# Performance work log

Hardware: AMD Instinct MI355X
Metric: run time of the kernel (lower is better)

## Reference

```python
import jax, jax.numpy as jnp
import numpy as np
import math

B, S, D = 1, 4096, 2048
H, KVH, HD = 16, 4, 128
ROPE_THETA = 10000.0


def _rope_tables(seq_len, head_dim, theta):
    inv_freq = 1.0 / (theta ** (jnp.arange(0, head_dim, 2, dtype=jnp.float32) / head_dim))
    t = jnp.arange(seq_len, dtype=jnp.float32)
    freqs = jnp.outer(t, inv_freq)                      # [S, HD/2]
    emb = jnp.concatenate([freqs, freqs], axis=-1)      # [S, HD]
    return jnp.cos(emb)[None, None], jnp.sin(emb)[None, None]  # [1,1,S,HD]


def setup_inputs() -> dict:
    key = jax.random.key(0)
    ks = jax.random.split(key, 8)
    hidden_states = jax.random.normal(ks[0], (B, S, D), dtype=jnp.float32)
    # additive causal mask [B,1,S,S]
    neg = jnp.finfo(jnp.float32).min
    causal = jnp.where(jnp.tril(jnp.ones((S, S), dtype=bool)), 0.0, neg)
    attention_mask = jnp.broadcast_to(causal[None, None], (B, 1, S, S)).astype(jnp.float32)
    cos, sin = _rope_tables(S, HD, ROPE_THETA)
    gate = jax.random.uniform(ks[1], (B, S), dtype=jnp.float32, minval=0.05, maxval=1.0)
    sc = lambda fan_in: 1.0 / math.sqrt(fan_in)
    Wq = jax.random.normal(ks[2], (D, H * HD), dtype=jnp.float32) * sc(D)
    Wk = jax.random.normal(ks[3], (D, KVH * HD), dtype=jnp.float32) * sc(D)
    Wv = jax.random.normal(ks[4], (D, KVH * HD), dtype=jnp.float32) * sc(D)
    Wo = jax.random.normal(ks[5], (H * HD, D), dtype=jnp.float32) * sc(H * HD)
    return {"hidden_states": hidden_states, "attention_mask": attention_mask,
            "cos": cos, "sin": sin, "gate": gate,
            "Wq": Wq, "Wk": Wk, "Wv": Wv, "Wo": Wo}


def _rotate_half(x):
    h = x.shape[-1] // 2
    return jnp.concatenate([-x[..., h:], x[..., :h]], axis=-1)


def reference(hidden_states, attention_mask, cos, sin, gate, Wq, Wk, Wv, Wo):
    bsz, q_len, _ = hidden_states.shape
    # projections -> [B, heads, S, HD]
    q = (hidden_states @ Wq).reshape(bsz, q_len, H, HD).transpose(0, 2, 1, 3)
    k = (hidden_states @ Wk).reshape(bsz, q_len, KVH, HD).transpose(0, 2, 1, 3)
    v = (hidden_states @ Wv).reshape(bsz, q_len, KVH, HD).transpose(0, 2, 1, 3)
    # inline RoPE
    q = q * cos + _rotate_half(q) * sin
    k = k * cos + _rotate_half(k) * sin
    # GQA: repeat-interleave kv heads to match q heads
    g = H // KVH
    k = jnp.repeat(k, g, axis=1)
    v = jnp.repeat(v, g, axis=1)
    scores = jnp.einsum('bhqd,bhkd->bhqk', q, k) / math.sqrt(HD)
    scores = scores + attention_mask
    scores = scores + jnp.log(gate + 1e-8)[:, None, None, :]  # gate over kv positions
    weights = jax.nn.softmax(scores.astype(jnp.float32), axis=-1).astype(q.dtype)
    out = jnp.einsum('bhqk,bhkd->bhqd', weights, v)
    out = out.transpose(0, 2, 1, 3).reshape(bsz, q_len, H * HD)
    return out @ Wo
```

## Files before the change

kernel.cpp:

```cpp
#include <hip/hip_runtime.h>
#include <math.h>

#define S_LEN 4096
#define DMODEL 2048
#define NH 16
#define NKVH 4
#define HD 128
#define LDQKV 3072

typedef __attribute__((ext_vector_type(4))) float f32x4;
typedef __attribute__((ext_vector_type(8))) short bf16x8;
typedef __attribute__((ext_vector_type(4))) unsigned short us4;

static __device__ __forceinline__ unsigned short f2bf(float f) {
  unsigned int u = __builtin_bit_cast(unsigned int, f);
  u += 0x7fffu + ((u >> 16) & 1u);
  return (unsigned short)(u >> 16);
}
static __device__ __forceinline__ float bf2f(unsigned short h) {
  unsigned int u = ((unsigned int)h) << 16;
  return __builtin_bit_cast(float, u);
}
static __device__ __forceinline__ unsigned int cvt_pk_bf16(float lo, float hi) {
  unsigned int r;
  asm("v_cvt_pk_bf16_f32 %0, %1, %2" : "=v"(r) : "v"(lo), "v"(hi));
  return r;
}

#define GLDS16(g, l) __builtin_amdgcn_global_load_lds( \
    (__attribute__((address_space(1))) void*)(g), \
    (__attribute__((address_space(3))) void*)(l), 16, 0, 0)


__global__ __launch_bounds__(256) void k_cast_bf16(const float* __restrict__ src,
                                                   unsigned short* __restrict__ dst, int n4) {
  int i = blockIdx.x * 256 + threadIdx.x;
  if (i >= n4) return;
  const float4* s = (const float4*)src;
  float4 v = s[i];
  us4 o = { f2bf(v.x), f2bf(v.y), f2bf(v.z), f2bf(v.w) };
  *(us4*)(dst + (size_t)i * 4) = o;
}

__global__ __launch_bounds__(256) void k_transpose_w(
    const float* __restrict__ Wq, const float* __restrict__ Wk,
    const float* __restrict__ Wv, const float* __restrict__ Wo,
    unsigned short* __restrict__ Wt, unsigned short* __restrict__ Wot) {
  __shared__ float tile[64][65];
  const int b = blockIdx.x;
  const float* src;
  unsigned short* dst;
  int N, c;
  if (b < 1024)      { src = Wq; dst = Wt;                         N = 2048; c = b; }
  else if (b < 1280) { src = Wk; dst = Wt + (size_t)2048 * 2048;   N = 512;  c = b - 1024; }
  else if (b < 1536) { src = Wv; dst = Wt + (size_t)2560 * 2048;   N = 512;  c = b - 1280; }
  else               { src = Wo; dst = Wot;                        N = 2048; c = b - 1536; }
  const int k0 = (c & 31) * 64, n0 = (c >> 5) * 64;
  const int t = threadIdx.x;
#pragma unroll
  for (int i = 0; i < 16; ++i) {
    int idx = t + i * 256;
    int r = idx >> 6, cc = idx & 63;
    tile[r][cc] = src[(size_t)(k0 + r) * N + n0 + cc];
  }
  __syncthreads();
#pragma unroll
  for (int i = 0; i < 16; ++i) {
    int idx = t + i * 256;
    int r = idx >> 6, cc = idx & 63;
    dst[(size_t)(n0 + r) * 2048 + k0 + cc] = f2bf(tile[cc][r]);
  }
}

__global__ __launch_bounds__(256) void k_rope_tv(unsigned short* __restrict__ QKV,
    const float* __restrict__ cp, const float* __restrict__ sp,
    unsigned short* __restrict__ Vt) {
  __shared__ unsigned short tile[64][72];
  const int b = blockIdx.x, t = threadIdx.x;
  if (b < 5120) {
    int gid = b * 256 + t;
    int d4 = (gid & 15) * 4;
    int hh = (gid >> 4) % 20;
    int s = gid / 320;
    int col = hh < NH ? hh * HD : DMODEL + (hh - NH) * HD;
    float qs = hh < NH ? 0.12751589341664477f : 1.0f;
    size_t base = (size_t)s * LDQKV + col + d4;
    us4 x1 = *(us4*)(QKV + base);
    us4 x2 = *(us4*)(QKV + base + 64);
    float4 c = *(const float4*)(cp + s * HD + d4);
    float4 sn = *(const float4*)(sp + s * HD + d4);
    us4 o1, o2;
    o1[0] = f2bf((bf2f(x1[0]) * c.x - bf2f(x2[0]) * sn.x) * qs);
    o1[1] = f2bf((bf2f(x1[1]) * c.y - bf2f(x2[1]) * sn.y) * qs);
    o1[2] = f2bf((bf2f(x1[2]) * c.z - bf2f(x2[2]) * sn.z) * qs);
    o1[3] = f2bf((bf2f(x1[3]) * c.w - bf2f(x2[3]) * sn.w) * qs);
    o2[0] = f2bf((bf2f(x2[0]) * c.x + bf2f(x1[0]) * sn.x) * qs);
    o2[1] = f2bf((bf2f(x2[1]) * c.y + bf2f(x1[1]) * sn.y) * qs);
    o2[2] = f2bf((bf2f(x2[2]) * c.z + bf2f(x1[2]) * sn.z) * qs);
    o2[3] = f2bf((bf2f(x2[3]) * c.w + bf2f(x1[3]) * sn.w) * qs);
    *(us4*)(QKV + base) = o1;
    *(us4*)(QKV + base + 64) = o2;
  } else {
    const int bb = b - 5120;
    const int s0 = (bb & 63) * 64, c0 = (bb >> 6) * 64;
#pragma unroll
    for (int i = 0; i < 16; ++i) {
      int idx = t + i * 256;
      int r = idx >> 6, cc = idx & 63;
      tile[r][cc] = QKV[(size_t)(s0 + r) * LDQKV + DMODEL + NKVH * HD + c0 + cc];
    }
    __syncthreads();
#pragma unroll
    for (int i = 0; i < 16; ++i) {
      int idx = t + i * 256;
      int r = idx >> 6, cc = idx & 63;
      int pc = (cc & 3) * 16 + (cc >> 2);
      Vt[(size_t)(c0 + r) * S_LEN + s0 + cc] = tile[pc][r];
    }
  }
}


template<int OUTF32>
__global__ __launch_bounds__(256) void k_gemm_bt(
    const unsigned short* __restrict__ A, const unsigned short* __restrict__ Bt,
    void* __restrict__ Cp, int M, int N, int K) {
  __shared__ __attribute__((aligned(16))) unsigned short As[128 * 32];
  __shared__ __attribute__((aligned(16))) unsigned short Bs[128 * 32];
  const int t = threadIdx.x;
  const int wave = t >> 6, lane = t & 63;
  const int lr = lane & 15, lg = lane >> 4;
  const int bm = blockIdx.x * 128, bn = blockIdx.y * 128;
  const int wr = (wave >> 1) * 64, wc = (wave & 1) * 64;
  f32x4 acc[4][4];
#pragma unroll
  for (int i = 0; i < 4; ++i)
#pragma unroll
    for (int j = 0; j < 4; ++j) acc[i][j] = (f32x4){0.f, 0.f, 0.f, 0.f};

  for (int k0 = 0; k0 < K; k0 += 32) {
    __syncthreads();
#pragma unroll
    for (int i = 0; i < 2; ++i) {
      const int cb = (wave * 2 + i) * 64;
      const int c = cb + lane;
      const int row = c >> 2, kc = c & 3;
      const int ksw = (kc ^ (row & 3)) * 8;
      GLDS16(A + (size_t)(bm + row) * K + k0 + ksw, (char*)As + cb * 16);
      GLDS16(Bt + (size_t)(bn + row) * K + k0 + ksw, (char*)Bs + cb * 16);
    }
    asm volatile("s_waitcnt vmcnt(0)" ::: "memory");
    __syncthreads();
    bf16x8 af[4], bfr[4];
#pragma unroll
    for (int mi = 0; mi < 4; ++mi) {
      const int row = wr + mi * 16 + lr;
      af[mi] = *(const bf16x8*)(As + row * 32 + ((lg ^ (lr & 3)) * 8));
    }
#pragma unroll
    for (int ni = 0; ni < 4; ++ni) {
      const int row = wc + ni * 16 + lr;
      bfr[ni] = *(const bf16x8*)(Bs + row * 32 + ((lg ^ (lr & 3)) * 8));
    }
#pragma unroll
    for (int mi = 0; mi < 4; ++mi)
#pragma unroll
      for (int ni = 0; ni < 4; ++ni)
        acc[mi][ni] = __builtin_amdgcn_mfma_f32_16x16x32_bf16(af[mi], bfr[ni], acc[mi][ni], 0, 0, 0);
  }
#pragma unroll
  for (int mi = 0; mi < 4; ++mi)
#pragma unroll
    for (int ni = 0; ni < 4; ++ni)
#pragma unroll
      for (int r = 0; r < 4; ++r) {
        const int m = bm + wr + mi * 16 + lg * 4 + r;
        const int n = bn + wc + ni * 16 + lr;
        if (OUTF32) ((float*)Cp)[(size_t)m * N + n] = acc[mi][ni][r];
        else ((unsigned short*)Cp)[(size_t)m * N + n] = f2bf(acc[mi][ni][r]);
      }
}


#define STAGE_KV(kt_, buf_) do { \
  const int kv0_ = (kt_) * 128; \
  _Pragma("unroll") \
  for (int i_ = 0; i_ < 4; ++i_) { \
    const int cb_ = (wave * 4 + i_) * 64; \
    const int c_ = cb_ + lane; \
    const int row_ = c_ >> 4, kc_ = c_ & 15; \
    const int sw_ = (kc_ ^ (row_ & 7)) * 8; \
    GLDS16(Kp + (size_t)(kv0_ + row_) * LDQKV + sw_, (char*)Ks[buf_] + cb_ * 16); \
    GLDS16(Vp + (size_t)row_ * S_LEN + kv0_ + sw_, (char*)Vs[buf_] + cb_ * 16); \
  } \
} while (0)

__device__ __forceinline__ void qkt_one(const unsigned short* Kb,
    const bf16x8* qf, f32x4* sc, int lr, int lg) {
  __builtin_amdgcn_s_setprio(1);
#pragma unroll
  for (int cf = 0; cf < 8; ++cf) {
    sc[cf] = (f32x4){0.f, 0.f, 0.f, 0.f};
    const int row = cf * 16 + lr;
#pragma unroll
    for (int ks = 0; ks < 4; ++ks) {
      bf16x8 kb = *(const bf16x8*)(Kb + row * 128 + (((ks * 4 + lg) ^ (lr & 7)) * 8));
      sc[cf] = __builtin_amdgcn_mfma_f32_16x16x32_bf16(qf[ks], kb, sc[cf], 0, 0, 0);
    }
  }
  __builtin_amdgcn_s_setprio(0);
}

template<bool DIAG>
__device__ __forceinline__ void softmax_pv(
    f32x4* sc, const unsigned short* Vb, unsigned short (*PsW)[72],
    const float* g8, int kv0, int qbase,
    f32x4* acc, f32x4& acc_s, float* mrow, int lr, int lg,
    const bf16x8 vb_ones) {
  if (DIAG) {
#pragma unroll
    for (int cf = 0; cf < 8; ++cf) {
      const int kpos = kv0 + cf * 16 + lr;
#pragma unroll
      for (int r = 0; r < 4; ++r)
        sc[cf][r] = (kpos <= qbase + r) ? sc[cf][r] : -3e38f;
    }
  }
  float lmax[4];
#pragma unroll
  for (int r = 0; r < 4; ++r) {
    float a = fmaxf(fmaxf(sc[0][r], sc[1][r]), fmaxf(sc[2][r], sc[3][r]));
    float b = fmaxf(fmaxf(sc[4][r], sc[5][r]), fmaxf(sc[6][r], sc[7][r]));
    lmax[r] = fmaxf(a, b);
  }
  bool need = (lmax[0] > mrow[0] + 11.5416f) | (lmax[1] > mrow[1] + 11.5416f) |
              (lmax[2] > mrow[2] + 11.5416f) | (lmax[3] > mrow[3] + 11.5416f);
  if (__any(need)) {
    float tm[4] = {lmax[0], lmax[1], lmax[2], lmax[3]};
#pragma unroll
    for (int off = 8; off; off >>= 1)
#pragma unroll
      for (int r = 0; r < 4; ++r) tm[r] = fmaxf(tm[r], __shfl_xor(tm[r], off));
#pragma unroll
    for (int r = 0; r < 4; ++r) {
      const float mn = fmaxf(mrow[r], tm[r]);
      const float alpha = __builtin_amdgcn_exp2f(mrow[r] - mn);
      mrow[r] = mn;
#pragma unroll
      for (int j = 0; j < 8; ++j) acc[j][r] *= alpha;
      acc_s[r] *= alpha;
    }
  }
#pragma unroll
  for (int hh = 0; hh < 2; ++hh) {
    const f32x4* s4 = sc + hh * 4;
    const float* g4 = g8 + hh * 4;
#pragma unroll
    for (int r = 0; r < 4; ++r) {
      float p0 = __builtin_amdgcn_exp2f(s4[0][r] - mrow[r]) * g4[0];
      float p1 = __builtin_amdgcn_exp2f(s4[1][r] - mrow[r]) * g4[1];
      float p2 = __builtin_amdgcn_exp2f(s4[2][r] - mrow[r]) * g4[2];
      float p3 = __builtin_amdgcn_exp2f(s4[3][r] - mrow[r]) * g4[3];
      uint2 pk = { cvt_pk_bf16(p0, p1), cvt_pk_bf16(p2, p3) };
      *(uint2*)(&PsW[lg * 4 + r][lr * 4]) = pk;
    }
    __builtin_amdgcn_s_setprio(1);
#pragma unroll
    for (int ks = 0; ks < 2; ++ks) {
      bf16x8 pa = *(const bf16x8*)(&PsW[lr][ks * 32 + lg * 8]);
#pragma unroll
      for (int j = 0; j < 8; ++j) {
        const int d = j * 16 + lr;
        bf16x8 vb = *(const bf16x8*)(Vb + d * 128 + ((hh * 8 + ((ks * 4 + lg) ^ (lr & 7))) * 8));
        acc[j] = __builtin_amdgcn_mfma_f32_16x16x32_bf16(pa, vb, acc[j], 0, 0, 0);
      }
      acc_s = __builtin_amdgcn_mfma_f32_16x16x32_bf16(pa, vb_ones, acc_s, 0, 0, 0);
    }
    __builtin_amdgcn_s_setprio(0);
  }
}

__global__ __launch_bounds__(512) void k_attn(
    const unsigned short* __restrict__ QKV, const unsigned short* __restrict__ Vt,
    const float* __restrict__ gate, unsigned short* __restrict__ Oattn) {
  __shared__ __attribute__((aligned(16))) unsigned short Ks[2][128 * 128];
  __shared__ __attribute__((aligned(16))) unsigned short Vs[2][128 * 128];
  __shared__ __attribute__((aligned(16))) unsigned short Ps[8][16][72];
  const int h = blockIdx.y, kvh = h >> 2;
  const int bx = blockIdx.x;
  const int t = threadIdx.x, wave = t >> 6, lane = t & 63;
  const int lr = lane & 15, lg = lane >> 4;
  const unsigned short* Qp = QKV + h * HD;
  const unsigned short* Kp = QKV + DMODEL + kvh * HD;
  const unsigned short* Vp = Vt + (size_t)kvh * HD * S_LEN;
  unsigned short (*PsW)[72] = Ps[wave];
  bf16x8 vb_ones;
  {
    const short one = (short)0x3F80, z = 0;
    const short e = (lr == 0) ? one : z;
    vb_ones = (bf16x8){e, e, e, e, e, e, e, e};
  }

  for (int half = 0; half < 2; ++half) {
    const int st = half ? bx : (31 - bx);
    const int q0 = st * 128;
    const int nt = st + 1;
    const int qbase = q0 + wave * 16 + lg * 4;

    bf16x8 qf[4];
    {
      const size_t qoff = (size_t)(q0 + wave * 16 + lr) * LDQKV;
#pragma unroll
      for (int ks = 0; ks < 4; ++ks)
        qf[ks] = *(const bf16x8*)(Qp + qoff + ks * 32 + lg * 8);
    }
    f32x4 acc[8];
#pragma unroll
    for (int j = 0; j < 8; ++j) acc[j] = (f32x4){0.f, 0.f, 0.f, 0.f};
    f32x4 acc_s = (f32x4){0.f, 0.f, 0.f, 0.f};
    float mrow[4] = {-3e38f, -3e38f, -3e38f, -3e38f};
    f32x4 sc[8];
    float g8[8];

    __builtin_amdgcn_s_barrier();
    STAGE_KV(0, 0);

    int kt = 0;
    for (; kt < nt - 1; ++kt) {
      STAGE_KV(kt + 1, (kt + 1) & 1);
      asm volatile("s_waitcnt vmcnt(8)" ::: "memory");
      __builtin_amdgcn_s_barrier();
#pragma unroll
      for (int cf = 0; cf < 8; ++cf) g8[cf] = gate[kt * 128 + cf * 16 + lr];
      qkt_one(Ks[kt & 1], qf, sc, lr, lg);
      softmax_pv<false>(sc, Vs[kt & 1], PsW, g8, kt * 128, qbase, acc, acc_s, mrow, lr, lg, vb_ones);
      __builtin_amdgcn_s_barrier();
    }
    {
      asm volatile("s_waitcnt vmcnt(0)" ::: "memory");
      __builtin_amdgcn_s_barrier();
#pragma unroll
      for (int cf = 0; cf < 8; ++cf) g8[cf] = gate[kt * 128 + cf * 16 + lr];
      qkt_one(Ks[kt & 1], qf, sc, lr, lg);
      softmax_pv<true>(sc, Vs[kt & 1], PsW, g8, kt * 128, qbase, acc, acc_s, mrow, lr, lg, vb_ones);
    }

    float inv[4];
#pragma unroll
    for (int r = 0; r < 4; ++r)
      inv[r] = 1.0f / __shfl(acc_s[r], lane & 48);
#pragma unroll
    for (int j = 0; j < 8; ++j)
#pragma unroll
      for (int r = 0; r < 4; ++r)
        Oattn[(size_t)(qbase + r) * DMODEL + h * HD + j * 16 + lr] = f2bf(acc[j][r] * inv[r]);
  }
}


extern "C" void kernel_launch(void* const* d_in, const int* in_sizes, int n_in,
                              void* d_out, int out_size, void* d_ws, size_t ws_size,
                              hipStream_t stream) {
  (void)in_sizes; (void)n_in; (void)out_size; (void)ws_size;
  const float* hid  = (const float*)d_in[0];
  const float* cosp = (const float*)d_in[2];
  const float* sinp = (const float*)d_in[3];
  const float* gate = (const float*)d_in[4];
  const float* Wq   = (const float*)d_in[5];
  const float* Wk   = (const float*)d_in[6];
  const float* Wv   = (const float*)d_in[7];
  const float* Wo   = (const float*)d_in[8];
  float* out = (float*)d_out;
  char* ws = (char*)d_ws;
  unsigned short* Xb   = (unsigned short*)(ws);
  unsigned short* Wt   = (unsigned short*)(ws + (size_t)16777216);
  unsigned short* Wot  = (unsigned short*)(ws + (size_t)29360128);
  unsigned short* QKV  = (unsigned short*)(ws + (size_t)37748736);
  unsigned short* Oatt = (unsigned short*)(ws + (size_t)62914560);
  unsigned short* Vt   = (unsigned short*)(ws + (size_t)79691776);

  k_cast_bf16<<<8192, 256, 0, stream>>>(hid, Xb, 2097152);
  k_transpose_w<<<2560, 256, 0, stream>>>(Wq, Wk, Wv, Wo, Wt, Wot);
  k_gemm_bt<0><<<dim3(32, 24), 256, 0, stream>>>(Xb, Wt, QKV, 4096, 3072, 2048);
  k_rope_tv<<<5632, 256, 0, stream>>>(QKV, cosp, sinp, Vt);
  k_attn<<<dim3(16, 16), 512, 0, stream>>>(QKV, Vt, gate, Oatt);
  k_gemm_bt<1><<<dim3(32, 16), 256, 0, stream>>>(Oatt, Wot, out, 4096, 2048, 2048);
}
```

Before: 260.0 us.

## Fuse RoPE into QKV GEMM epilogue, merge prep kernels, reshape GEMM wave tiling

Applies RoPE and the query scale inside the QKV projection GEMM epilogue. To make this possible, each wave now owns a 32x128 strip, so both rotary halves of a head sit in the same wave's accumulators. The cast and weight-transpose kernels are merged into one launch, and the V-transpose becomes its own small kernel. This removes one full read-modify-write pass over the Q/K region and one kernel launch. The cost is a different MFMA tiling (2x8 fragments per wave, with more B-fragment LDS reads per wave) and uncoalesced cos/sin loads in the epilogue.

Measured after the change: 248.5 us. 1.05x faster.

```diff
diff --git a/kernel.cpp b/kernel.cpp
--- a/kernel.cpp
+++ b/kernel.cpp
@@ -32,31 +32,30 @@
     (__attribute__((address_space(3))) void*)(l), 16, 0, 0)
 
 
-__global__ __launch_bounds__(256) void k_cast_bf16(const float* __restrict__ src,
-                                                   unsigned short* __restrict__ dst, int n4) {
-  int i = blockIdx.x * 256 + threadIdx.x;
-  if (i >= n4) return;
-  const float4* s = (const float4*)src;
-  float4 v = s[i];
-  us4 o = { f2bf(v.x), f2bf(v.y), f2bf(v.z), f2bf(v.w) };
-  *(us4*)(dst + (size_t)i * 4) = o;
-}
-
-__global__ __launch_bounds__(256) void k_transpose_w(
+__global__ __launch_bounds__(256) void k_prep(
+    const float* __restrict__ hid, unsigned short* __restrict__ Xb,
     const float* __restrict__ Wq, const float* __restrict__ Wk,
     const float* __restrict__ Wv, const float* __restrict__ Wo,
     unsigned short* __restrict__ Wt, unsigned short* __restrict__ Wot) {
   __shared__ float tile[64][65];
-  const int b = blockIdx.x;
+  const int b = blockIdx.x, t = threadIdx.x;
+  if (b < 8192) {
+    int i = b * 256 + t;
+    const float4* s = (const float4*)hid;
+    float4 v = s[i];
+    us4 o = { f2bf(v.x), f2bf(v.y), f2bf(v.z), f2bf(v.w) };
+    *(us4*)(Xb + (size_t)i * 4) = o;
+    return;
+  }
+  const int bb = b - 8192;
   const float* src;
   unsigned short* dst;
   int N, c;
-  if (b < 1024)      { src = Wq; dst = Wt;                         N = 2048; c = b; }
-  else if (b < 1280) { src = Wk; dst = Wt + (size_t)2048 * 2048;   N = 512;  c = b - 1024; }
-  else if (b < 1536) { src = Wv; dst = Wt + (size_t)2560 * 2048;   N = 512;  c = b - 1280; }
-  else               { src = Wo; dst = Wot;                        N = 2048; c = b - 1536; }
+  if (bb < 1024)      { src = Wq; dst = Wt;                       N = 2048; c = bb; }
+  else if (bb < 1280) { src = Wk; dst = Wt + (size_t)2048 * 2048; N = 512;  c = bb - 1024; }
+  else if (bb < 1536) { src = Wv; dst = Wt + (size_t)2560 * 2048; N = 512;  c = bb - 1280; }
+  else                { src = Wo; dst = Wot;                      N = 2048; c = bb - 1536; }
   const int k0 = (c & 31) * 64, n0 = (c >> 5) * 64;
-  const int t = threadIdx.x;
 #pragma unroll
   for (int i = 0; i < 16; ++i) {
     int idx = t + i * 256;
@@ -72,71 +71,46 @@
   }
 }
 
-__global__ __launch_bounds__(256) void k_rope_tv(unsigned short* __restrict__ QKV,
-    const float* __restrict__ cp, const float* __restrict__ sp,
-    unsigned short* __restrict__ Vt) {
+
+__global__ __launch_bounds__(256) void k_vt(
+    const unsigned short* __restrict__ QKV, unsigned short* __restrict__ Vt) {
   __shared__ unsigned short tile[64][72];
   const int b = blockIdx.x, t = threadIdx.x;
-  if (b < 5120) {
-    int gid = b * 256 + t;
-    int d4 = (gid & 15) * 4;
-    int hh = (gid >> 4) % 20;
-    int s = gid / 320;
-    int col = hh < NH ? hh * HD : DMODEL + (hh - NH) * HD;
-    float qs = hh < NH ? 0.12751589341664477f : 1.0f;
-    size_t base = (size_t)s * LDQKV + col + d4;
-    us4 x1 = *(us4*)(QKV + base);
-    us4 x2 = *(us4*)(QKV + base + 64);
-    float4 c = *(const float4*)(cp + s * HD + d4);
-    float4 sn = *(const float4*)(sp + s * HD + d4);
-    us4 o1, o2;
-    o1[0] = f2bf((bf2f(x1[0]) * c.x - bf2f(x2[0]) * sn.x) * qs);
-    o1[1] = f2bf((bf2f(x1[1]) * c.y - bf2f(x2[1]) * sn.y) * qs);
-    o1[2] = f2bf((bf2f(x1[2]) * c.z - bf2f(x2[2]) * sn.z) * qs);
-    o1[3] = f2bf((bf2f(x1[3]) * c.w - bf2f(x2[3]) * sn.w) * qs);
-    o2[0] = f2bf((bf2f(x2[0]) * c.x + bf2f(x1[0]) * sn.x) * qs);
-    o2[1] = f2bf((bf2f(x2[1]) * c.y + bf2f(x1[1]) * sn.y) * qs);
-    o2[2] = f2bf((bf2f(x2[2]) * c.z + bf2f(x1[2]) * sn.z) * qs);
-    o2[3] = f2bf((bf2f(x2[3]) * c.w + bf2f(x1[3]) * sn.w) * qs);
-    *(us4*)(QKV + base) = o1;
-    *(us4*)(QKV + base + 64) = o2;
-  } else {
-    const int bb = b - 5120;
-    const int s0 = (bb & 63) * 64, c0 = (bb >> 6) * 64;
-#pragma unroll
-    for (int i = 0; i < 16; ++i) {
-      int idx = t + i * 256;
-      int r = idx >> 6, cc = idx & 63;
-      tile[r][cc] = QKV[(size_t)(s0 + r) * LDQKV + DMODEL + NKVH * HD + c0 + cc];
-    }
-    __syncthreads();
-#pragma unroll
-    for (int i = 0; i < 16; ++i) {
-      int idx = t + i * 256;
-      int r = idx >> 6, cc = idx & 63;
-      int pc = (cc & 3) * 16 + (cc >> 2);
-      Vt[(size_t)(c0 + r) * S_LEN + s0 + cc] = tile[pc][r];
-    }
-  }
-}
-
-
-template<int OUTF32>
+  const int s0 = (b & 63) * 64, c0 = (b >> 6) * 64;
+#pragma unroll
+  for (int i = 0; i < 16; ++i) {
+    int idx = t + i * 256;
+    int r = idx >> 6, cc = idx & 63;
+    tile[r][cc] = QKV[(size_t)(s0 + r) * LDQKV + DMODEL + NKVH * HD + c0 + cc];
+  }
+  __syncthreads();
+#pragma unroll
+  for (int i = 0; i < 16; ++i) {
+    int idx = t + i * 256;
+    int r = idx >> 6, cc = idx & 63;
+    int pc = (cc & 3) * 16 + (cc >> 2);
+    Vt[(size_t)(c0 + r) * S_LEN + s0 + cc] = tile[pc][r];
+  }
+}
+
+
+template<int MODE>
 __global__ __launch_bounds__(256) void k_gemm_bt(
     const unsigned short* __restrict__ A, const unsigned short* __restrict__ Bt,
-    void* __restrict__ Cp, int M, int N, int K) {
+    void* __restrict__ Cp, int M, int N, int K,
+    const float* __restrict__ cp, const float* __restrict__ sp) {
   __shared__ __attribute__((aligned(16))) unsigned short As[128 * 32];
   __shared__ __attribute__((aligned(16))) unsigned short Bs[128 * 32];
   const int t = threadIdx.x;
   const int wave = t >> 6, lane = t & 63;
   const int lr = lane & 15, lg = lane >> 4;
   const int bm = blockIdx.x * 128, bn = blockIdx.y * 128;
-  const int wr = (wave >> 1) * 64, wc = (wave & 1) * 64;
-  f32x4 acc[4][4];
-#pragma unroll
-  for (int i = 0; i < 4; ++i)
-#pragma unroll
-    for (int j = 0; j < 4; ++j) acc[i][j] = (f32x4){0.f, 0.f, 0.f, 0.f};
+  const int wr = wave * 32;
+  f32x4 acc[2][8];
+#pragma unroll
+  for (int i = 0; i < 2; ++i)
+#pragma unroll
+    for (int j = 0; j < 8; ++j) acc[i][j] = (f32x4){0.f, 0.f, 0.f, 0.f};
 
   for (int k0 = 0; k0 < K; k0 += 32) {
     __syncthreads();
@@ -151,32 +125,52 @@
     }
     asm volatile("s_waitcnt vmcnt(0)" ::: "memory");
     __syncthreads();
-    bf16x8 af[4], bfr[4];
-#pragma unroll
-    for (int mi = 0; mi < 4; ++mi) {
+    bf16x8 af[2], bfr[8];
+#pragma unroll
+    for (int mi = 0; mi < 2; ++mi) {
       const int row = wr + mi * 16 + lr;
       af[mi] = *(const bf16x8*)(As + row * 32 + ((lg ^ (lr & 3)) * 8));
     }
 #pragma unroll
-    for (int ni = 0; ni < 4; ++ni) {
-      const int row = wc + ni * 16 + lr;
+    for (int ni = 0; ni < 8; ++ni) {
+      const int row = ni * 16 + lr;
       bfr[ni] = *(const bf16x8*)(Bs + row * 32 + ((lg ^ (lr & 3)) * 8));
     }
 #pragma unroll
-    for (int mi = 0; mi < 4; ++mi)
-#pragma unroll
-      for (int ni = 0; ni < 4; ++ni)
+    for (int mi = 0; mi < 2; ++mi)
+#pragma unroll
+      for (int ni = 0; ni < 8; ++ni)
         acc[mi][ni] = __builtin_amdgcn_mfma_f32_16x16x32_bf16(af[mi], bfr[ni], acc[mi][ni], 0, 0, 0);
   }
-#pragma unroll
-  for (int mi = 0; mi < 4; ++mi)
-#pragma unroll
-    for (int ni = 0; ni < 4; ++ni)
+
+  if (MODE == 1 && bn < NKVH * HD + DMODEL) {
+    const float qs = bn < DMODEL ? 0.12751589341664477f : 1.0f;
+    unsigned short* o = (unsigned short*)Cp;
+#pragma unroll
+    for (int mi = 0; mi < 2; ++mi)
 #pragma unroll
       for (int r = 0; r < 4; ++r) {
         const int m = bm + wr + mi * 16 + lg * 4 + r;
-        const int n = bn + wc + ni * 16 + lr;
-        if (OUTF32) ((float*)Cp)[(size_t)m * N + n] = acc[mi][ni][r];
+#pragma unroll
+        for (int ni = 0; ni < 4; ++ni) {
+          const int d = ni * 16 + lr;
+          const float c = cp[m * HD + d], s = sp[m * HD + d];
+          const float x1 = acc[mi][ni][r], x2 = acc[mi][ni + 4][r];
+          o[(size_t)m * N + bn + d]      = f2bf((x1 * c - x2 * s) * qs);
+          o[(size_t)m * N + bn + d + 64] = f2bf((x2 * c + x1 * s) * qs);
+        }
+      }
+    return;
+  }
+#pragma unroll
+  for (int mi = 0; mi < 2; ++mi)
+#pragma unroll
+    for (int ni = 0; ni < 8; ++ni)
+#pragma unroll
+      for (int r = 0; r < 4; ++r) {
+        const int m = bm + wr + mi * 16 + lg * 4 + r;
+        const int n = bn + ni * 16 + lr;
+        if (MODE == 2) ((float*)Cp)[(size_t)m * N + n] = acc[mi][ni][r];
         else ((unsigned short*)Cp)[(size_t)m * N + n] = f2bf(acc[mi][ni][r]);
       }
 }
@@ -379,10 +373,9 @@
   unsigned short* Oatt = (unsigned short*)(ws + (size_t)62914560);
   unsigned short* Vt   = (unsigned short*)(ws + (size_t)79691776);
 
-  k_cast_bf16<<<8192, 256, 0, stream>>>(hid, Xb, 2097152);
-  k_transpose_w<<<2560, 256, 0, stream>>>(Wq, Wk, Wv, Wo, Wt, Wot);
-  k_gemm_bt<0><<<dim3(32, 24), 256, 0, stream>>>(Xb, Wt, QKV, 4096, 3072, 2048);
-  k_rope_tv<<<5632, 256, 0, stream>>>(QKV, cosp, sinp, Vt);
+  k_prep<<<10752, 256, 0, stream>>>(hid, Xb, Wq, Wk, Wv, Wo, Wt, Wot);
+  k_gemm_bt<1><<<dim3(32, 24), 256, 0, stream>>>(Xb, Wt, QKV, 4096, 3072, 2048, cosp, sinp);
+  k_vt<<<512, 256, 0, stream>>>(QKV, Vt);
   k_attn<<<dim3(16, 16), 512, 0, stream>>>(QKV, Vt, gate, Oatt);
-  k_gemm_bt<1><<<dim3(32, 16), 256, 0, stream>>>(Oatt, Wot, out, 4096, 2048, 2048);
-}
+  k_gemm_bt<2><<<dim3(32, 16), 256, 0, stream>>>(Oatt, Wot, out, 4096, 2048, 2048, nullptr, nullptr);
+}
```
